# Performance work log

Hardware: AMD Instinct MI355X
Metric: run time of the kernel (lower is better)

The kernel has to match this reference:

```python
import jax, jax.numpy as jnp
import numpy as np

EPS_NORM = 1e-12
BN_EPS = 1e-5

def rmsnorm(x, gamma):
    # F.normalize(x, dim=-1) * gamma * dim**0.5
    n = jnp.maximum(jnp.linalg.norm(x, axis=-1, keepdims=True), EPS_NORM)
    return x / n * gamma * np.float32(np.sqrt(x.shape[-1]))

def conv1d(x, w, pad):
    # x: (B,C,T), w: (O,I,K)
    return jax.lax.conv_general_dilated(x, w, (1,), [(pad, pad)],
                                        dimension_numbers=('NCH', 'OIH', 'NCH'))

def maxpool3(x):
    # kernel 3, stride 1, pad 1 over last axis
    return jax.lax.reduce_window(x, -jnp.inf, jax.lax.max,
                                 (1, 1, 3), (1, 1, 1), [(0, 0), (0, 0), (1, 1)])

def gelu(x):
    return jax.nn.gelu(x, approximate=False)  # matches torch F.gelu default


def setup_inputs() -> dict:
    key = jax.random.key(0)
    ks = jax.random.split(key, 16)
    B, N, D, E, H, NF = 4, 4096, 512, 4, 1024, 32
    s = 0.02
    inp = {
        'x': jax.random.normal(ks[0], (B, N, D), jnp.float32),
        'left_k': 2048,
        'gamma1': jnp.ones((D,), jnp.float32),
        'gamma2': jnp.ones((D,), jnp.float32),
        'attn_w': jax.random.normal(ks[1], (D, 1), jnp.float32) * s,
        'attn_b': jnp.zeros((1,), jnp.float32),
        'gate_w': jax.random.normal(ks[2], (D, E), jnp.float32) * s,
        'expert_w1': jax.random.normal(ks[3], (E, D, H), jnp.float32) * s,
        'expert_w2': jax.random.normal(ks[4], (E, H, D), jnp.float32) * s,
        'bott_w': jax.random.normal(ks[5], (NF, D, 1), jnp.float32) * s,
        'conv_w39': jax.random.normal(ks[6], (NF, NF, 39), jnp.float32) * s,
        'conv_w19': jax.random.normal(ks[7], (NF, NF, 19), jnp.float32) * s,
        'conv_w9': jax.random.normal(ks[8], (NF, NF, 9), jnp.float32) * s,
        'mp_w': jax.random.normal(ks[9], (NF, D, 1), jnp.float32) * s,
        'bn_g': jnp.ones((NF * 4,), jnp.float32),
        'bn_b': jnp.zeros((NF * 4,), jnp.float32),
        'proj_w': jax.random.normal(ks[10], (NF * 4, D), jnp.float32) * s,
        'proj_b': jnp.zeros((D,), jnp.float32),
    }
    return inp


def reference(x, left_k, gamma1, gamma2, attn_w, attn_b, gate_w,
              expert_w1, expert_w2, bott_w, conv_w39, conv_w19, conv_w9,
              mp_w, bn_g, bn_b, proj_w, proj_b):
    B, N, D = x.shape
    E = gate_w.shape[-1]

    x_n = rmsnorm(x, gamma1)
    scores = jax.nn.sigmoid(x_n @ attn_w + attn_b)            # (B,N,1)
    xs = x_n * scores                                          # (B,N,D)

    # top-k token selection (remain_ratio < 1 path)
    _, top_idx = jax.lax.top_k(scores[..., 0], left_k)         # (B,left_k)
    sorted_idx = jnp.sort(top_idx, axis=1)
    left_x = jnp.take_along_axis(xs, sorted_idx[..., None], axis=1)
    # complement sum via scatter mask (faithful to scatter_/gather/sum)
    sel = jnp.zeros((B, N), x.dtype).at[jnp.arange(B)[:, None], sorted_idx].set(1.0)
    extra = jnp.einsum('bn,bnd->bd', 1.0 - sel, xs)[:, None, :]
    xcat = jnp.concatenate([left_x, extra], axis=1)            # (B,left_k+1,D)

    x_n2 = rmsnorm(xcat, gamma2)

    # dense soft MoE
    gate = jax.nn.softmax(x_n2 @ gate_w, axis=-1)              # (B,T,E)
    h = gelu(jnp.einsum('btd,edh->bteh', x_n2, expert_w1))
    eo = jnp.einsum('bteh,ehd->bted', h, expert_w2)
    moe_out = jnp.einsum('bte,bted->btd', gate, eo)
    moe_loss = E * jnp.sum(jnp.mean(gate, axis=(0, 1)) ** 2)

    # Inception branch (channels-first)
    xc = jnp.transpose(x_n2, (0, 2, 1))                        # (B,D,T)
    xb = conv1d(xc, bott_w, 0)                                 # (B,32,T)
    outs = [conv1d(xb, conv_w39, 19), conv1d(xb, conv_w19, 9),
            conv1d(xb, conv_w9, 4), conv1d(maxpool3(xc), mp_w, 0)]
    cat = jnp.concatenate(outs, axis=1)                        # (B,128,T)
    mu = jnp.mean(cat, axis=(0, 2), keepdims=True)
    var = jnp.var(cat, axis=(0, 2), keepdims=True)
    bn = (cat - mu) / jnp.sqrt(var + BN_EPS) * bn_g[None, :, None] + bn_b[None, :, None]
    incep = gelu(bn)
    incep_out = jnp.transpose(incep, (0, 2, 1)) @ proj_w + proj_b  # (B,T,D)

    out = xcat + moe_out + incep_out
    return gelu(out), moe_loss
```

## Files before the change

kernel.cpp:

```cpp
#include <hip/hip_runtime.h>
#include <hip/hip_bf16.h>
#include <math.h>

#define DEV __device__ __forceinline__

constexpr int B_ = 4, N_ = 4096, D_ = 512, E_ = 4, H_ = 1024, NF_ = 32;
constexpr int KL_ = 2048, T_ = KL_ + 1;
constexpr int TOK_ = B_ * T_;
constexpr int SP_ = 2304;

typedef __bf16 bf16x8 __attribute__((ext_vector_type(8)));
typedef float f32x4 __attribute__((ext_vector_type(4)));

DEV float gelu_f(float x){
  float t = __expf(-1.702f * x);
  return x * __builtin_amdgcn_rcpf(1.0f + t);
}
DEV float bf2f(unsigned short u){ union{unsigned int i; float f;} c; c.i = (unsigned)u << 16; return c.f; }
DEV unsigned pack2(float a, float b){
  __hip_bfloat16 ha = __float2bfloat16(a), hb = __float2bfloat16(b);
  unsigned short ua = *(unsigned short*)&ha, ub = *(unsigned short*)&hb;
  return (unsigned)ua | ((unsigned)ub << 16);
}

DEV float wave_sum(float v){
  #pragma unroll
  for (int off = 32; off > 0; off >>= 1) v += __shfl_down(v, off, 64);
  return v;
}

DEV float block_sum256(float v, float* sm){
  v = wave_sum(v);
  int lane = threadIdx.x & 63, wid = threadIdx.x >> 6;
  if (lane == 0) sm[wid] = v;
  __syncthreads();
  if (threadIdx.x == 0) sm[0] = sm[0] + sm[1] + sm[2] + sm[3];
  __syncthreads();
  float r = sm[0];
  __syncthreads();
  return r;
}

__global__ void k_rms_score(const float* __restrict__ x, const float* __restrict__ g,
                            const float* __restrict__ aw, const float* __restrict__ ab,
                            float* __restrict__ scores, float* __restrict__ scale){
  __shared__ float sm[4];
  int row = blockIdx.x; int tid = threadIdx.x;
  const float* xr = x + (size_t)row * D_;
  float v0 = xr[tid], v1 = xr[tid + 256];
  float ss = block_sum256(v0 * v0 + v1 * v1, sm);
  float a  = block_sum256(v0 * g[tid] * aw[tid] + v1 * g[tid + 256] * aw[tid + 256], sm);
  float n = fmaxf(sqrtf(ss), 1e-12f);
  float inv = 22.627416997969522f / n;
  float z = inv * a + ab[0];
  float s = 1.0f / (1.0f + expf(-z));
  if (tid == 0){ scores[row] = s; scale[row] = inv * s; }
}

__global__ void k_select(const float* __restrict__ scores, int* __restrict__ flags){
  __shared__ float s[N_];
  __shared__ int cnts[4][64];
  int b = blockIdx.y; int tid = threadIdx.x;
  int tile = blockIdx.x * 64;
  const float4* src = (const float4*)(scores + (size_t)b * N_);
  for (int j = tid; j < N_ / 4; j += 256) ((float4*)s)[j] = src[j];
  __syncthreads();
  int tok = tid & 63, part = tid >> 6;
  int i = tile + tok;
  float si = s[i];
  int cnt = 0;
  const float4* sp = (const float4*)(s + part * 1024);
  int jb = part * 1024;
  #pragma unroll 4
  for (int j = 0; j < 256; j++){
    float4 v = sp[j];
    int j4 = jb + j * 4;
    cnt += (v.x > si) || (v.x == si && (j4 + 0) < i);
    cnt += (v.y > si) || (v.y == si && (j4 + 1) < i);
    cnt += (v.z > si) || (v.z == si && (j4 + 2) < i);
    cnt += (v.w > si) || (v.w == si && (j4 + 3) < i);
  }
  cnts[part][tok] = cnt;
  __syncthreads();
  if (tid < 64){
    int c = cnts[0][tid] + cnts[1][tid] + cnts[2][tid] + cnts[3][tid];
    flags[(size_t)b * N_ + tile + tid] = (c < KL_) ? 1 : 0;
  }
}

__global__ void k_compact(const int* __restrict__ flags, int* __restrict__ idx){
  __shared__ int wsum[4];
  int b = blockIdx.x; int tid = threadIdx.x;
  const int* fb = flags + (size_t)b * N_;
  int f[16]; int cnt = 0;
  #pragma unroll
  for (int i = 0; i < 16; i++){ f[i] = fb[tid * 16 + i]; cnt += f[i]; }
  int lane = tid & 63, wid = tid >> 6;
  int v = cnt;
  #pragma unroll
  for (int off = 1; off < 64; off <<= 1){
    int t = __shfl_up(v, off, 64);
    if (lane >= off) v += t;
  }
  if (lane == 63) wsum[wid] = v;
  __syncthreads();
  int base = v - cnt;
  for (int w = 0; w < wid; w++) base += wsum[w];
  int* ib = idx + (size_t)b * KL_;
  #pragma unroll
  for (int i = 0; i < 16; i++){
    if (f[i]) ib[base++] = tid * 16 + i;
  }
}

DEV void rms2_tail(int row, float xc0, float xc1,
                   const float* __restrict__ g2, const float* __restrict__ gw,
                   __hip_bfloat16* __restrict__ xcatb,
                   __hip_bfloat16* __restrict__ xn2b, float* __restrict__ gate,
                   float* sm, float* sg){
  int tid = threadIdx.x;
  __hip_bfloat16* xb = xcatb + (size_t)row * D_;
  xb[tid] = __float2bfloat16(xc0); xb[tid + 256] = __float2bfloat16(xc1);
  float ss = block_sum256(xc0 * xc0 + xc1 * xc1, sm);
  float n = fmaxf(sqrtf(ss), 1e-12f);
  float inv = 22.627416997969522f / n;
  float xn0 = xc0 * inv * g2[tid], xn1 = xc1 * inv * g2[tid + 256];
  __hip_bfloat16* ob = xn2b + (size_t)row * D_;
  ob[tid] = __float2bfloat16(xn0); ob[tid + 256] = __float2bfloat16(xn1);
  const float4* gw4 = (const float4*)gw;
  float4 wa = gw4[tid], wb = gw4[tid + 256];
  float l0 = xn0 * wa.x + xn1 * wb.x, l1 = xn0 * wa.y + xn1 * wb.y;
  float l2 = xn0 * wa.z + xn1 * wb.z, l3 = xn0 * wa.w + xn1 * wb.w;
  l0 = wave_sum(l0); l1 = wave_sum(l1); l2 = wave_sum(l2); l3 = wave_sum(l3);
  int lane = tid & 63, wid = tid >> 6;
  if (lane == 0){ sg[wid*4+0]=l0; sg[wid*4+1]=l1; sg[wid*4+2]=l2; sg[wid*4+3]=l3; }
  __syncthreads();
  if (tid == 0){
    float a0 = sg[0]+sg[4]+sg[8]+sg[12];
    float a1 = sg[1]+sg[5]+sg[9]+sg[13];
    float a2 = sg[2]+sg[6]+sg[10]+sg[14];
    float a3 = sg[3]+sg[7]+sg[11]+sg[15];
    float m = fmaxf(fmaxf(a0, a1), fmaxf(a2, a3));
    float e0 = expf(a0-m), e1 = expf(a1-m), e2 = expf(a2-m), e3 = expf(a3-m);
    float is = 1.f / (e0+e1+e2+e3);
    float* gr = gate + (size_t)row * 4;
    gr[0]=e0*is; gr[1]=e1*is; gr[2]=e2*is; gr[3]=e3*is;
  }
}

__global__ void k_gatherrms(const float* __restrict__ x, const float* __restrict__ scale,
                            const float* __restrict__ g1, const float* __restrict__ g2,
                            const float* __restrict__ gw, const int* __restrict__ idx,
                            __hip_bfloat16* __restrict__ xcatb,
                            __hip_bfloat16* __restrict__ xn2b, float* __restrict__ gate){
  __shared__ float sm[4];
  __shared__ float sg[16];
  int rid = blockIdx.x;
  int b = rid >> 11, p = rid & (KL_ - 1);
  int tid = threadIdx.x;
  int tok = idx[(size_t)b * KL_ + p];
  float sc = scale[(size_t)b * N_ + tok];
  const float* xr = x + ((size_t)b * N_ + tok) * D_;
  float xc0 = xr[tid] * sc * g1[tid];
  float xc1 = xr[tid + 256] * sc * g1[tid + 256];
  rms2_tail(b * T_ + p, xc0, xc1, g2, gw, xcatb, xn2b, gate, sm, sg);
}

__global__ void k_extra1(const float* __restrict__ x, const float* __restrict__ scale,
                         const int* __restrict__ flags, float* __restrict__ part){
  int b = blockIdx.y, blk = blockIdx.x;
  int tid = threadIdx.x;
  const int* fb = flags + (size_t)b * N_ + blk * 64;
  const float* sb = scale + (size_t)b * N_ + blk * 64;
  const float2* xp = (const float2*)(x + ((size_t)b * N_ + blk * 64) * D_) + tid;
  float2 acc = {0.f, 0.f};
  for (int i = 0; i < 64; i++){
    if (!fb[i]){
      float s = sb[i];
      float2 v = xp[(size_t)i * 256];
      acc.x += v.x * s; acc.y += v.y * s;
    }
  }
  float* pr = part + ((size_t)(b * 64 + blk)) * D_;
  pr[tid * 2] = acc.x; pr[tid * 2 + 1] = acc.y;
}

__global__ void k_extra2r(const float* __restrict__ part, const float* __restrict__ g1,
                          const float* __restrict__ g2, const float* __restrict__ gw,
                          __hip_bfloat16* __restrict__ xcatb,
                          __hip_bfloat16* __restrict__ xn2b, float* __restrict__ gate){
  __shared__ float sm[4];
  __shared__ float sg[16];
  int b = blockIdx.x; int tid = threadIdx.x;
  float s0 = 0.f, s1 = 0.f;
  for (int i = 0; i < 64; i++){
    const float* pr = part + ((size_t)(b * 64 + i)) * D_;
    s0 += pr[tid]; s1 += pr[tid + 256];
  }
  float xc0 = s0 * g1[tid], xc1 = s1 * g1[tid + 256];
  rms2_tail(b * T_ + KL_, xc0, xc1, g2, gw, xcatb, xn2b, gate, sm, sg);
}

__global__ void k_gsumloss(const float* __restrict__ gate, float* __restrict__ o){
  __shared__ float sm[16];
  int tid = threadIdx.x;
  float4 a = {0.f, 0.f, 0.f, 0.f};
  for (int r = tid; r < TOK_; r += 256){
    float4 v = *(const float4*)(gate + (size_t)r * 4);
    a.x += v.x; a.y += v.y; a.z += v.z; a.w += v.w;
  }
  a.x = wave_sum(a.x); a.y = wave_sum(a.y); a.z = wave_sum(a.z); a.w = wave_sum(a.w);
  int lane = tid & 63, wid = tid >> 6;
  if (lane == 0){ sm[wid*4]=a.x; sm[wid*4+1]=a.y; sm[wid*4+2]=a.z; sm[wid*4+3]=a.w; }
  __syncthreads();
  if (tid == 0){
    float l = 0.f;
    #pragma unroll
    for (int e = 0; e < 4; e++){
      float s = sm[e] + sm[4+e] + sm[8+e] + sm[12+e];
      float m = s / (float)TOK_;
      l += m * m;
    }
    o[0] = (float)E_ * l;
  }
}

DEV void trb_tile(const float* __restrict__ in, __hip_bfloat16* __restrict__ out,
                  int R, int C, int bx, int by){
  __shared__ float t[32][33];
  int c0 = bx * 32, r0 = by * 32;
  int j = threadIdx.x & 31, i4 = threadIdx.x >> 5;
  #pragma unroll
  for (int k = 0; k < 4; k++){
    int i = i4 * 4 + k;
    t[i][j] = in[(size_t)(r0 + i) * C + c0 + j];
  }
  __syncthreads();
  #pragma unroll
  for (int k = 0; k < 4; k++){
    int i = i4 * 4 + k;
    out[(size_t)(c0 + i) * R + r0 + j] = __float2bfloat16(t[j][i]);
  }
}

__global__ void k_wprep(const float* __restrict__ ew1, const float* __restrict__ ew2,
                        const float* __restrict__ proj_w,
                        const float* __restrict__ w39, const float* __restrict__ w19,
                        const float* __restrict__ w9,
                        __hip_bfloat16* __restrict__ w1b, __hip_bfloat16* __restrict__ w2b,
                        __hip_bfloat16* __restrict__ projb, __hip_bfloat16* __restrict__ wcb,
                        float* __restrict__ stats){
  int blk = blockIdx.x;
  int tid = threadIdx.x;
  if (blk < 2048){
    int e = blk >> 9, rem = blk & 511;
    int by = rem >> 5, bx = rem & 31;
    trb_tile(ew1 + (size_t)e * D_ * H_, w1b + (size_t)e * D_ * H_, D_, H_, bx, by);
  } else if (blk < 4096){
    int r = blk - 2048;
    int e = r >> 9, r2 = r & 511;
    int bx = r2 & 15, by = r2 >> 4;
    __shared__ float t[32][33];
    const float* ip = ew2 + (size_t)e * H_ * D_;
    __hip_bfloat16* op = w2b + (size_t)e * H_;
    int c0 = bx * 32, r0 = by * 32;
    int j = tid & 31, i4 = tid >> 5;
    #pragma unroll
    for (int k = 0; k < 4; k++){
      int i = i4 * 4 + k;
      t[i][j] = ip[(size_t)(r0 + i) * D_ + c0 + j];
    }
    __syncthreads();
    #pragma unroll
    for (int k = 0; k < 4; k++){
      int i = i4 * 4 + k;
      int v = r0 + j;
      int pv = (v & ~63) | ((v & 15) << 2) | ((v >> 4) & 3);
      op[(size_t)(c0 + i) * 4096 + pv] = __float2bfloat16(t[j][i]);
    }
  } else if (blk < 4160){
    int r = blk - 4096;
    trb_tile(proj_w, projb, 128, D_, r & 15, r >> 4);
  } else if (blk < 4448){
    int i = (blk - 4160) * 256 + tid;
    if (i < 73728){
      const float* w; int KP, KW, base;
      if (i < 40960){ w = w39; KP = 40; KW = 39; base = 0; }
      else if (i < 61440){ w = w19; KP = 20; KW = 19; base = 40960; }
      else { w = w9; KP = 12; KW = 9; base = 61440; }
      int li = i - base;
      int oc = li / (32 * KP);
      int rem = li % (32 * KP);
      int k = rem >> 5, ic = rem & 31;
      float v = (k < KW) ? w[((size_t)oc * 32 + ic) * KW + k] : 0.f;
      wcb[i] = __float2bfloat16(v);
    }
  } else {
    stats[tid] = 0.f;
  }
}

template<int EPI>
__launch_bounds__(512)
__global__ void gemm_bt(const __hip_bfloat16* __restrict__ A,
                        const __hip_bfloat16* __restrict__ Bt,
                        __hip_bfloat16* __restrict__ Cb, size_t zstride,
                        int M, int N, int K, int kloc,
                        const float* __restrict__ gatep){
  __shared__ __align__(16) char smem[2][24576];
  int tid = threadIdx.x;
  unsigned gx = gridDim.x;
  unsigned nwg = gx * gridDim.y;
  unsigned orig = blockIdx.x + gx * blockIdx.y;
  unsigned q = nwg >> 3, r = nwg & 7;
  unsigned xcd = orig & 7, loc = orig >> 3;
  unsigned wg = (xcd < r ? xcd * (q + 1) : r * (q + 1) + (xcd - r) * q) + loc;
  int m0 = (int)(wg / gx) * 256, n0 = (int)(wg % gx) * 128;
  int z = blockIdx.z;
  int koff = z * kloc;
  int ln = tid & 63, wid = tid >> 6;
  int wm = wid >> 1, wn = wid & 1;

  f32x4 acc[4][4] = {};

  auto stage = [&](int buf, int k0){
    #pragma unroll
    for (int c = 0; c < 2; c++){
      int ii = tid + c * 512;
      int rr = ii >> 2, s = ii & 3;
      int gm = m0 + rr; gm = gm < M ? gm : M - 1;
      const __hip_bfloat16* gp = A + (size_t)gm * K + (koff + k0 + ((s ^ (rr & 3)) << 3));
      __builtin_amdgcn_global_load_lds(
          (const __attribute__((address_space(1))) void*)gp,
          (__attribute__((address_space(3))) void*)&smem[buf][ii * 16], 16, 0, 0);
    }
    {
      int ii = tid;
      int rr = ii >> 2, s = ii & 3;
      const __hip_bfloat16* gp = Bt + (size_t)(n0 + rr) * K + (koff + k0 + ((s ^ (rr & 3)) << 3));
      __builtin_amdgcn_global_load_lds(
          (const __attribute__((address_space(1))) void*)gp,
          (__attribute__((address_space(3))) void*)&smem[buf][16384 + ii * 16], 16, 0, 0);
    }
  };

  int nk = kloc >> 5;
  stage(0, 0);
  __syncthreads();
  int slotb = (((ln >> 4) ^ (ln & 3)) << 4);
  for (int t = 0; t < nk; t++){
    int buf = t & 1;
    if (t + 1 < nk) stage(buf ^ 1, (t + 1) << 5);
    bf16x8 af[4], bfr[4];
    #pragma unroll
    for (int m = 0; m < 4; m++){
      int R = wm * 64 + m * 16 + (ln & 15);
      af[m] = *(const bf16x8*)&smem[buf][R * 64 + slotb];
    }
    #pragma unroll
    for (int n = 0; n < 4; n++){
      int R = wn * 64 + n * 16 + (ln & 15);
      bfr[n] = *(const bf16x8*)&smem[buf][16384 + R * 64 + slotb];
    }
    #pragma unroll
    for (int m = 0; m < 4; m++)
      #pragma unroll
      for (int n = 0; n < 4; n++)
        acc[m][n] = __builtin_amdgcn_mfma_f32_16x16x32_bf16(af[m], bfr[n], acc[m][n], 0, 0, 0);
    __syncthreads();
  }

  __hip_bfloat16* Co = Cb + (size_t)z * zstride;
  int e = n0 >> 10;
  int lr = ln & 15;
  #pragma unroll
  for (int m = 0; m < 4; m++){
    int rb = m0 + wm * 64 + m * 16 + ((ln >> 4) << 2);
    float gv[4];
    if (EPI == 1){
      #pragma unroll
      for (int r2 = 0; r2 < 4; r2++)
        gv[r2] = (rb + r2 < M) ? gatep[(size_t)(rb + r2) * 4 + e] : 0.f;
    }
    #pragma unroll
    for (int r2 = 0; r2 < 4; r2++){
      int row = rb + r2;
      if (row < M){
        float v0 = acc[m][0][r2], v1 = acc[m][1][r2];
        float v2 = acc[m][2][r2], v3 = acc[m][3][r2];
        if (EPI == 1){
          v0 = gelu_f(v0) * gv[r2]; v1 = gelu_f(v1) * gv[r2];
          v2 = gelu_f(v2) * gv[r2]; v3 = gelu_f(v3) * gv[r2];
        }
        uint2 pk; pk.x = pack2(v0, v1); pk.y = pack2(v2, v3);
        size_t ci = (size_t)row * N + (n0 + wn * 64 + 4 * lr);
        *(uint2*)&Co[ci] = pk;
      }
    }
  }
}

__global__ void k_1x1F(const __hip_bfloat16* __restrict__ xn2b, const float* __restrict__ bw,
                       const float* __restrict__ mw,
                       __hip_bfloat16* __restrict__ xbp, float* __restrict__ cat){
  __shared__ float Xs[32 * 65];
  __shared__ float Ws[64 * 36];
  int type = blockIdx.y;
  const float* w = type == 0 ? bw : mw;
  int tid = threadIdx.x;
  int G0 = blockIdx.x * 32;
  int tok = tid & 31, grp = tid >> 5;
  float acc[4] = {};
  for (int d0 = 0; d0 < D_; d0 += 64){
    #pragma unroll
    for (int j = tid; j < 512; j += 256){
      int tt = j >> 4, dc = (j & 15) * 4;
      int g = G0 + tt;
      float4 v = {0.f, 0.f, 0.f, 0.f};
      if (g < TOK_){
        const __hip_bfloat16* p = xn2b + (size_t)g * D_ + d0 + dc;
        ushort4 rw = *(const ushort4*)p;
        v.x = bf2f(rw.x); v.y = bf2f(rw.y); v.z = bf2f(rw.z); v.w = bf2f(rw.w);
        if (type == 1){
          int t = g % T_;
          if (t > 0){
            ushort4 u = *(const ushort4*)(p - D_);
            v.x = fmaxf(v.x, bf2f(u.x)); v.y = fmaxf(v.y, bf2f(u.y));
            v.z = fmaxf(v.z, bf2f(u.z)); v.w = fmaxf(v.w, bf2f(u.w));
          }
          if (t < T_ - 1){
            ushort4 u = *(const ushort4*)(p + D_);
            v.x = fmaxf(v.x, bf2f(u.x)); v.y = fmaxf(v.y, bf2f(u.y));
            v.z = fmaxf(v.z, bf2f(u.z)); v.w = fmaxf(v.w, bf2f(u.w));
          }
        }
      }
      float* xd = &Xs[tt * 65 + dc];
      xd[0] = v.x; xd[1] = v.y; xd[2] = v.z; xd[3] = v.w;
    }
    #pragma unroll
    for (int j = tid; j < 2048; j += 256){
      int f = j >> 6, d = j & 63;
      Ws[d * 36 + f] = w[(size_t)f * D_ + d0 + d];
    }
    __syncthreads();
    const float* xr = &Xs[tok * 65];
    #pragma unroll 8
    for (int d = 0; d < 64; d++){
      float xv = xr[d];
      const float4* w4 = (const float4*)&Ws[d * 36 + grp * 4];
      float4 a = w4[0];
      acc[0] += xv * a.x; acc[1] += xv * a.y; acc[2] += xv * a.z; acc[3] += xv * a.w;
    }
    __syncthreads();
  }
  int g = G0 + tok;
  if (g < TOK_){
    if (type == 0){
      int bb = g / T_, t = g % T_;
      __hip_bfloat16* op = xbp + ((size_t)(bb * SP_ + 32 + t)) * 32 + grp * 4;
      #pragma unroll
      for (int j = 0; j < 4; j++) op[j] = __float2bfloat16(acc[j]);
    } else {
      float* op = cat + (size_t)g * 128 + 96 + grp * 4;
      #pragma unroll
      for (int j = 0; j < 4; j++) op[j] = acc[j];
    }
  }
}

template<int KP, int PAD, int OFF, int TYPE>
DEV void convm_body(const __hip_bfloat16* __restrict__ xbp,
                    const __hip_bfloat16* __restrict__ wcb,
                    float* __restrict__ cat, char* smem){
  constexpr int R = KP * 32;
  int t0 = blockIdx.x * 128, b = blockIdx.y;
  int tid = threadIdx.x;
  for (int j = tid; j < 768; j += 256){
    int r = j >> 2, c = j & 3;
    int rg = b * SP_ + 32 + t0 - PAD + r;
    const __hip_bfloat16* gp = xbp + (size_t)rg * 32 + ((c ^ (r & 3)) << 3);
    __builtin_amdgcn_global_load_lds(
        (const __attribute__((address_space(1))) void*)gp,
        (__attribute__((address_space(3))) void*)(smem + j * 16), 16, 0, 0);
  }
  __syncthreads();
  int ln = tid & 63, wid = tid >> 6;
  int lr = ln & 15, lg = ln >> 4;
  int tb = wid * 32;
  const __hip_bfloat16* wt = wcb + OFF;
  const __hip_bfloat16* bp0 = wt + (size_t)lr * R + lg * 8;
  const __hip_bfloat16* bp1 = wt + (size_t)(16 + lr) * R + lg * 8;
  f32x4 acc[2][2] = {};
  bf16x8 bc0 = *(const bf16x8*)bp0;
  bf16x8 bc1 = *(const bf16x8*)bp1;
  #pragma unroll 4
  for (int s = 0; s < KP; s++){
    bf16x8 bn0 = bc0, bn1 = bc1;
    if (s + 1 < KP){
      bn0 = *(const bf16x8*)(bp0 + (s + 1) * 32);
      bn1 = *(const bf16x8*)(bp1 + (s + 1) * 32);
    }
    int ra0 = tb + lr + s;
    int ra1 = tb + 16 + lr + s;
    bf16x8 a0 = *(const bf16x8*)(smem + ra0 * 64 + ((lg ^ (ra0 & 3)) << 4));
    bf16x8 a1 = *(const bf16x8*)(smem + ra1 * 64 + ((lg ^ (ra1 & 3)) << 4));
    acc[0][0] = __builtin_amdgcn_mfma_f32_16x16x32_bf16(a0, bc0, acc[0][0], 0, 0, 0);
    acc[0][1] = __builtin_amdgcn_mfma_f32_16x16x32_bf16(a0, bc1, acc[0][1], 0, 0, 0);
    acc[1][0] = __builtin_amdgcn_mfma_f32_16x16x32_bf16(a1, bc0, acc[1][0], 0, 0, 0);
    acc[1][1] = __builtin_amdgcn_mfma_f32_16x16x32_bf16(a1, bc1, acc[1][1], 0, 0, 0);
    bc0 = bn0; bc1 = bn1;
  }
  #pragma unroll
  for (int m = 0; m < 2; m++){
    int rb = tb + m * 16 + (lg << 2);
    #pragma unroll
    for (int n = 0; n < 2; n++){
      int oc = n * 16 + lr;
      #pragma unroll
      for (int j2 = 0; j2 < 4; j2++){
        int tp = t0 + rb + j2;
        if (tp < T_)
          cat[((size_t)b * T_ + tp) * 128 + TYPE * 32 + oc] = acc[m][n][j2];
      }
    }
  }
}

__global__ __launch_bounds__(256)
void k_convM(const __hip_bfloat16* __restrict__ xbp,
             const __hip_bfloat16* __restrict__ wcb, float* __restrict__ cat){
  __shared__ __align__(16) char smem[192 * 64];
  if (blockIdx.z == 0)      convm_body<40, 19, 0,     0>(xbp, wcb, cat, smem);
  else if (blockIdx.z == 1) convm_body<20, 9,  40960, 1>(xbp, wcb, cat, smem);
  else                      convm_body<12, 4,  61440, 2>(xbp, wcb, cat, smem);
}

__global__ void k_bnstat(const float* __restrict__ cat, float* __restrict__ stats){
  __shared__ float sm[512];
  int tid = threadIdx.x;
  float s = 0.f, q = 0.f;
  for (int rp = blockIdx.x; rp < TOK_ / 2; rp += gridDim.x){
    float v = cat[(size_t)rp * 256 + tid];
    s += v; q += v * v;
  }
  sm[tid] = s; sm[256 + tid] = q;
  __syncthreads();
  if (tid < 128){
    atomicAdd(&stats[tid], sm[tid] + sm[tid + 128]);
    atomicAdd(&stats[128 + tid], sm[256 + tid] + sm[256 + tid + 128]);
  }
}

__global__ void k_bnact(const float* __restrict__ cat, __hip_bfloat16* __restrict__ catb,
                        const float* __restrict__ stats,
                        const float* __restrict__ g, const float* __restrict__ b){
  int i = blockIdx.x * 256 + threadIdx.x;
  int c = i & 127;
  float mu = stats[c] * (1.f / TOK_);
  float var = stats[128 + c] * (1.f / TOK_) - mu * mu;
  float v = cat[i];
  v = (v - mu) * rsqrtf(var + 1e-5f) * g[c] + b[c];
  catb[i] = __float2bfloat16(gelu_f(v));
}

__global__ void k_final(const __hip_bfloat16* __restrict__ xcatb,
                        const __hip_bfloat16* __restrict__ moeb,
                        size_t zs, const __hip_bfloat16* __restrict__ ioutb,
                        const float* __restrict__ pb, float* __restrict__ out){
  size_t i = ((size_t)blockIdx.x * 256 + threadIdx.x) * 2;
  int p = (int)(i & 511);
  size_t rowbase = i - p;
  float s0 = 0.f, s1 = 0.f;
  #pragma unroll
  for (int z = 0; z < 4; z++){
    unsigned u = *(const unsigned*)&moeb[(size_t)z * zs + i];
    s0 += bf2f((unsigned short)(u & 0xffff));
    s1 += bf2f((unsigned short)(u >> 16));
  }
  unsigned v = *(const unsigned*)&ioutb[i];
  s0 += bf2f((unsigned short)(v & 0xffff));
  s1 += bf2f((unsigned short)(v >> 16));
  int d0 = (p & ~63) | ((p & 3) << 4) | ((p >> 2) & 15);
  int p1 = p + 1;
  int d1 = (p1 & ~63) | ((p1 & 3) << 4) | ((p1 >> 2) & 15);
  const unsigned short* xc = (const unsigned short*)xcatb;
  s0 += bf2f(xc[rowbase + d0]) + pb[d0];
  s1 += bf2f(xc[rowbase + d1]) + pb[d1];
  out[rowbase + d0] = gelu_f(s0);
  out[rowbase + d1] = gelu_f(s1);
}

extern "C" void kernel_launch(void* const* d_in, const int* in_sizes, int n_in,
                              void* d_out, int out_size, void* d_ws, size_t ws_size,
                              hipStream_t stream){
  const float* x      = (const float*)d_in[0];
  const float* gamma1 = (const float*)d_in[2];
  const float* gamma2 = (const float*)d_in[3];
  const float* attn_w = (const float*)d_in[4];
  const float* attn_b = (const float*)d_in[5];
  const float* gate_w = (const float*)d_in[6];
  const float* ew1    = (const float*)d_in[7];
  const float* ew2    = (const float*)d_in[8];
  const float* bott_w = (const float*)d_in[9];
  const float* w39    = (const float*)d_in[10];
  const float* w19    = (const float*)d_in[11];
  const float* w9     = (const float*)d_in[12];
  const float* mp_w   = (const float*)d_in[13];
  const float* bn_g   = (const float*)d_in[14];
  const float* bn_b   = (const float*)d_in[15];
  const float* proj_w = (const float*)d_in[16];
  const float* proj_b = (const float*)d_in[17];
  float* out = (float*)d_out;

  float* ws = (float*)d_ws;
  size_t off = 0;
  auto alloc = [&](size_t n){ size_t o = off; off += (n + 63) & ~(size_t)63; return o; };
  size_t f_hb   = alloc((size_t)TOK_ * 4096 / 2);
  size_t f_sc   = alloc(B_ * N_);
  size_t f_sca  = alloc(B_ * N_);
  size_t f_fl   = alloc(B_ * N_);
  size_t f_idx  = alloc(B_ * KL_);
  size_t f_xcb  = alloc((size_t)TOK_ * D_ / 2 + 64);
  size_t f_moeb = alloc((size_t)4 * TOK_ * D_ / 2 + 64);
  size_t f_gate = alloc(TOK_ * E_);
  size_t f_st   = alloc(256);
  size_t f_xbp  = alloc((size_t)B_ * SP_ * 32 / 2);
  size_t f_cat  = alloc((size_t)TOK_ * 128);
  size_t f_wb   = alloc((size_t)(E_ * D_ * H_) + (size_t)TOK_ * D_ / 2 + 64);
  size_t f_part = alloc((size_t)B_ * 64 * D_);
  size_t f_wcb  = alloc(73728 / 2 + 64);
  size_t f_pjb  = alloc(512 * 128 / 2 + 64);
  (void)ws_size; (void)in_sizes; (void)n_in; (void)out_size;

  float* sc   = ws + f_sc;
  float* sca  = ws + f_sca;
  int*   fl   = (int*)(ws + f_fl);
  int*   idx  = (int*)(ws + f_idx);
  float* gate = ws + f_gate;
  float* stats= ws + f_st;
  float* cat  = ws + f_cat;
  float* part = ws + f_part;
  __hip_bfloat16* xcatb = (__hip_bfloat16*)(ws + f_xcb);
  __hip_bfloat16* moeb  = (__hip_bfloat16*)(ws + f_moeb);
  __hip_bfloat16* xbp   = (__hip_bfloat16*)(ws + f_xbp);
  __hip_bfloat16* wcb   = (__hip_bfloat16*)(ws + f_wcb);
  __hip_bfloat16* projb = (__hip_bfloat16*)(ws + f_pjb);
  __hip_bfloat16* hbuf  = (__hip_bfloat16*)(ws + f_hb);
  __hip_bfloat16* ioutb = (__hip_bfloat16*)(ws + f_hb);
  __hip_bfloat16* catb  = (__hip_bfloat16*)(ws + f_hb + 4196416);
  __hip_bfloat16* w1b  = (__hip_bfloat16*)(ws + f_wb);
  __hip_bfloat16* w2b  = w1b + (size_t)E_ * D_ * H_;
  __hip_bfloat16* xn2b = w2b + (size_t)E_ * D_ * H_;

  hipMemsetAsync(xbp, 0, (size_t)B_ * SP_ * 32 * sizeof(__hip_bfloat16), stream);

  k_wprep<<<4449, 256, 0, stream>>>(ew1, ew2, proj_w, w39, w19, w9,
                                    w1b, w2b, projb, wcb, stats);

  k_rms_score<<<B_ * N_, 256, 0, stream>>>(x, gamma1, attn_w, attn_b, sc, sca);
  k_select<<<dim3(N_ / 64, B_), 256, 0, stream>>>(sc, fl);
  k_compact<<<B_, 256, 0, stream>>>(fl, idx);
  k_gatherrms<<<B_ * KL_, 256, 0, stream>>>(x, sca, gamma1, gamma2, gate_w, idx,
                                            xcatb, xn2b, gate);
  k_extra1<<<dim3(64, B_), 256, 0, stream>>>(x, sca, fl, part);
  k_extra2r<<<B_, 256, 0, stream>>>(part, gamma1, gamma2, gate_w, xcatb, xn2b, gate);
  k_gsumloss<<<1, 256, 0, stream>>>(gate, out + (size_t)TOK_ * D_);

  int mt = (TOK_ + 255) / 256;
  size_t zs = (size_t)TOK_ * D_;
  gemm_bt<1><<<dim3(4096/128, mt), 512, 0, stream>>>(
      xn2b, w1b, hbuf, 0, TOK_, 4096, D_, D_, gate);
  gemm_bt<0><<<dim3(D_/128, mt, 4), 512, 0, stream>>>(
      hbuf, w2b, moeb, zs, TOK_, D_, 4096, 1024, nullptr);

  int t32 = (TOK_ + 31) / 32;
  k_1x1F<<<dim3(t32, 2), 256, 0, stream>>>(xn2b, bott_w, mp_w, xbp, cat);
  k_convM<<<dim3(17, 4, 3), 256, 0, stream>>>(xbp, wcb, cat);
  k_bnstat<<<256, 256, 0, stream>>>(cat, stats);
  k_bnact<<<(TOK_ * 128) / 256, 256, 0, stream>>>(cat, catb, stats, bn_g, bn_b);
  gemm_bt<0><<<dim3(D_/128, mt), 512, 0, stream>>>(
      catb, projb, ioutb, 0, TOK_, D_, 128, 128, nullptr);
  k_final<<<((size_t)TOK_ * D_) / 512, 256, 0, stream>>>(xcatb, moeb, zs, ioutb, proj_b, out);
}
```

Baseline: 297.3 us.

## Move 1x1 bottleneck and maxpool convs onto MFMA with separate pool kernel

Replaces the scalar fp32 shared-memory 1x1 conv kernel with a bf16 MFMA kernel that double-buffers 128-token tiles through LDS via direct global-to-LDS loads. The 3-wide maxpool is split into its own kernel that writes a pooled bf16 copy of the normalized input, and the 1x1 weights are pre-converted to bf16 in the weight-prep kernel. This targets the FMA-bound scalar loop. In exchange it adds an extra launch and a full activation-sized round trip through memory for the pooled tensor.

```diff
diff --git a/kernel.cpp b/kernel.cpp
--- a/kernel.cpp
+++ b/kernel.cpp
@@ -247,9 +247,10 @@
                         const float* __restrict__ proj_w,
                         const float* __restrict__ w39, const float* __restrict__ w19,
                         const float* __restrict__ w9,
+                        const float* __restrict__ bott_w, const float* __restrict__ mp_w,
                         __hip_bfloat16* __restrict__ w1b, __hip_bfloat16* __restrict__ w2b,
                         __hip_bfloat16* __restrict__ projb, __hip_bfloat16* __restrict__ wcb,
-                        float* __restrict__ stats){
+                        __hip_bfloat16* __restrict__ wb1x1, float* __restrict__ stats){
   int blk = blockIdx.x;
   int tid = threadIdx.x;
   if (blk < 2048){
@@ -295,6 +296,10 @@
       float v = (k < KW) ? w[((size_t)oc * 32 + ic) * KW + k] : 0.f;
       wcb[i] = __float2bfloat16(v);
     }
+  } else if (blk < 4576){
+    int i = (blk - 4448) * 256 + tid;
+    const float* w = (i < 16384) ? bott_w : mp_w;
+    wb1x1[i] = __float2bfloat16(w[i & 16383]);
   } else {
     stats[tid] = 0.f;
   }
@@ -400,71 +405,94 @@
   }
 }
 
-__global__ void k_1x1F(const __hip_bfloat16* __restrict__ xn2b, const float* __restrict__ bw,
-                       const float* __restrict__ mw,
-                       __hip_bfloat16* __restrict__ xbp, float* __restrict__ cat){
-  __shared__ float Xs[32 * 65];
-  __shared__ float Ws[64 * 36];
+__global__ void k_pool(const unsigned* __restrict__ xin, unsigned* __restrict__ xout){
+  size_t i = (size_t)blockIdx.x * 256 + threadIdx.x;
+  if (i >= (size_t)TOK_ * 256) return;
+  int g = (int)(i >> 8);
+  int t = g % T_;
+  unsigned c = xin[i];
+  float a0 = bf2f((unsigned short)(c & 0xffff)), a1 = bf2f((unsigned short)(c >> 16));
+  if (t > 0){
+    unsigned u = xin[i - 256];
+    a0 = fmaxf(a0, bf2f((unsigned short)(u & 0xffff)));
+    a1 = fmaxf(a1, bf2f((unsigned short)(u >> 16)));
+  }
+  if (t < T_ - 1){
+    unsigned u = xin[i + 256];
+    a0 = fmaxf(a0, bf2f((unsigned short)(u & 0xffff)));
+    a1 = fmaxf(a1, bf2f((unsigned short)(u >> 16)));
+  }
+  xout[i] = pack2(a0, a1);
+}
+
+__global__ __launch_bounds__(256)
+void k_1x1M(const __hip_bfloat16* __restrict__ xn2b, const __hip_bfloat16* __restrict__ xn2mb,
+            const __hip_bfloat16* __restrict__ wb1x1,
+            __hip_bfloat16* __restrict__ xbp, float* __restrict__ cat){
+  __shared__ __align__(16) char smem[2][16384];
   int type = blockIdx.y;
-  const float* w = type == 0 ? bw : mw;
-  int tid = threadIdx.x;
-  int G0 = blockIdx.x * 32;
-  int tok = tid & 31, grp = tid >> 5;
-  float acc[4] = {};
-  for (int d0 = 0; d0 < D_; d0 += 64){
-    #pragma unroll
-    for (int j = tid; j < 512; j += 256){
-      int tt = j >> 4, dc = (j & 15) * 4;
-      int g = G0 + tt;
-      float4 v = {0.f, 0.f, 0.f, 0.f};
-      if (g < TOK_){
-        const __hip_bfloat16* p = xn2b + (size_t)g * D_ + d0 + dc;
-        ushort4 rw = *(const ushort4*)p;
-        v.x = bf2f(rw.x); v.y = bf2f(rw.y); v.z = bf2f(rw.z); v.w = bf2f(rw.w);
-        if (type == 1){
-          int t = g % T_;
-          if (t > 0){
-            ushort4 u = *(const ushort4*)(p - D_);
-            v.x = fmaxf(v.x, bf2f(u.x)); v.y = fmaxf(v.y, bf2f(u.y));
-            v.z = fmaxf(v.z, bf2f(u.z)); v.w = fmaxf(v.w, bf2f(u.w));
-          }
-          if (t < T_ - 1){
-            ushort4 u = *(const ushort4*)(p + D_);
-            v.x = fmaxf(v.x, bf2f(u.x)); v.y = fmaxf(v.y, bf2f(u.y));
-            v.z = fmaxf(v.z, bf2f(u.z)); v.w = fmaxf(v.w, bf2f(u.w));
+  const __hip_bfloat16* A = type ? xn2mb : xn2b;
+  const __hip_bfloat16* W = wb1x1 + (size_t)type * 32 * 512;
+  int t0 = blockIdx.x * 128;
+  int tid = threadIdx.x, ln = tid & 63, wid = tid >> 6;
+  int lr = ln & 15, lg = ln >> 4;
+
+  auto stage = [&](int buf, int k0){
+    #pragma unroll
+    for (int c = 0; c < 4; c++){
+      int ii = tid + c * 256;
+      int r = ii >> 3, s = ii & 7;
+      int row = t0 + r; row = row < TOK_ ? row : TOK_ - 1;
+      const __hip_bfloat16* gp = A + (size_t)row * D_ + k0 + ((s ^ (r & 7)) << 3);
+      __builtin_amdgcn_global_load_lds(
+          (const __attribute__((address_space(1))) void*)gp,
+          (__attribute__((address_space(3))) void*)&smem[buf][ii * 16], 16, 0, 0);
+    }
+  };
+
+  f32x4 acc[2][2] = {};
+  stage(0, 0);
+  __syncthreads();
+  for (int t = 0; t < 8; t++){
+    int buf = t & 1;
+    if (t + 1 < 8) stage(buf ^ 1, (t + 1) * 64);
+    int k0 = t * 64;
+    #pragma unroll
+    for (int kk = 0; kk < 2; kk++){
+      bf16x8 bfr[2];
+      #pragma unroll
+      for (int n = 0; n < 2; n++)
+        bfr[n] = *(const bf16x8*)&W[(size_t)(n * 16 + lr) * 512 + k0 + kk * 32 + lg * 8];
+      #pragma unroll
+      for (int m = 0; m < 2; m++){
+        int R = wid * 32 + m * 16 + lr;
+        int phys = (kk * 4 + lg) ^ (R & 7);
+        bf16x8 af = *(const bf16x8*)&smem[buf][R * 128 + phys * 16];
+        acc[m][0] = __builtin_amdgcn_mfma_f32_16x16x32_bf16(af, bfr[0], acc[m][0], 0, 0, 0);
+        acc[m][1] = __builtin_amdgcn_mfma_f32_16x16x32_bf16(af, bfr[1], acc[m][1], 0, 0, 0);
+      }
+    }
+    __syncthreads();
+  }
+  #pragma unroll
+  for (int m = 0; m < 2; m++){
+    int rb = t0 + wid * 32 + m * 16 + lg * 4;
+    #pragma unroll
+    for (int n = 0; n < 2; n++){
+      int oc = n * 16 + lr;
+      #pragma unroll
+      for (int r2 = 0; r2 < 4; r2++){
+        int g = rb + r2;
+        if (g < TOK_){
+          float v = acc[m][n][r2];
+          if (type == 0){
+            int bb = g / T_, t = g % T_;
+            xbp[((size_t)(bb * SP_ + 32 + t)) * 32 + oc] = __float2bfloat16(v);
+          } else {
+            cat[(size_t)g * 128 + 96 + oc] = v;
           }
         }
       }
-      float* xd = &Xs[tt * 65 + dc];
-      xd[0] = v.x; xd[1] = v.y; xd[2] = v.z; xd[3] = v.w;
-    }
-    #pragma unroll
-    for (int j = tid; j < 2048; j += 256){
-      int f = j >> 6, d = j & 63;
-      Ws[d * 36 + f] = w[(size_t)f * D_ + d0 + d];
-    }
-    __syncthreads();
-    const float* xr = &Xs[tok * 65];
-    #pragma unroll 8
-    for (int d = 0; d < 64; d++){
-      float xv = xr[d];
-      const float4* w4 = (const float4*)&Ws[d * 36 + grp * 4];
-      float4 a = w4[0];
-      acc[0] += xv * a.x; acc[1] += xv * a.y; acc[2] += xv * a.z; acc[3] += xv * a.w;
-    }
-    __syncthreads();
-  }
-  int g = G0 + tok;
-  if (g < TOK_){
-    if (type == 0){
-      int bb = g / T_, t = g % T_;
-      __hip_bfloat16* op = xbp + ((size_t)(bb * SP_ + 32 + t)) * 32 + grp * 4;
-      #pragma unroll
-      for (int j = 0; j < 4; j++) op[j] = __float2bfloat16(acc[j]);
-    } else {
-      float* op = cat + (size_t)g * 128 + 96 + grp * 4;
-      #pragma unroll
-      for (int j = 0; j < 4; j++) op[j] = acc[j];
     }
   }
 }
@@ -626,11 +654,13 @@
   size_t f_gate = alloc(TOK_ * E_);
   size_t f_st   = alloc(256);
   size_t f_xbp  = alloc((size_t)B_ * SP_ * 32 / 2);
+  size_t f_xmb  = alloc((size_t)TOK_ * D_ / 2 + 64);
   size_t f_cat  = alloc((size_t)TOK_ * 128);
   size_t f_wb   = alloc((size_t)(E_ * D_ * H_) + (size_t)TOK_ * D_ / 2 + 64);
   size_t f_part = alloc((size_t)B_ * 64 * D_);
   size_t f_wcb  = alloc(73728 / 2 + 64);
   size_t f_pjb  = alloc(512 * 128 / 2 + 64);
+  size_t f_w11  = alloc(32768 / 2 + 64);
   (void)ws_size; (void)in_sizes; (void)n_in; (void)out_size;
 
   float* sc   = ws + f_sc;
@@ -644,8 +674,10 @@
   __hip_bfloat16* xcatb = (__hip_bfloat16*)(ws + f_xcb);
   __hip_bfloat16* moeb  = (__hip_bfloat16*)(ws + f_moeb);
   __hip_bfloat16* xbp   = (__hip_bfloat16*)(ws + f_xbp);
+  __hip_bfloat16* xn2mb = (__hip_bfloat16*)(ws + f_xmb);
   __hip_bfloat16* wcb   = (__hip_bfloat16*)(ws + f_wcb);
   __hip_bfloat16* projb = (__hip_bfloat16*)(ws + f_pjb);
+  __hip_bfloat16* wb1x1 = (__hip_bfloat16*)(ws + f_w11);
   __hip_bfloat16* hbuf  = (__hip_bfloat16*)(ws + f_hb);
   __hip_bfloat16* ioutb = (__hip_bfloat16*)(ws + f_hb);
   __hip_bfloat16* catb  = (__hip_bfloat16*)(ws + f_hb + 4196416);
@@ -655,8 +687,8 @@
 
   hipMemsetAsync(xbp, 0, (size_t)B_ * SP_ * 32 * sizeof(__hip_bfloat16), stream);
 
-  k_wprep<<<4449, 256, 0, stream>>>(ew1, ew2, proj_w, w39, w19, w9,
-                                    w1b, w2b, projb, wcb, stats);
+  k_wprep<<<4577, 256, 0, stream>>>(ew1, ew2, proj_w, w39, w19, w9, bott_w, mp_w,
+                                    w1b, w2b, projb, wcb, wb1x1, stats);
 
   k_rms_score<<<B_ * N_, 256, 0, stream>>>(x, gamma1, attn_w, attn_b, sc, sca);
   k_select<<<dim3(N_ / 64, B_), 256, 0, stream>>>(sc, fl);
@@ -674,8 +706,9 @@
   gemm_bt<0><<<dim3(D_/128, mt, 4), 512, 0, stream>>>(
       hbuf, w2b, moeb, zs, TOK_, D_, 4096, 1024, nullptr);
 
-  int t32 = (TOK_ + 31) / 32;
-  k_1x1F<<<dim3(t32, 2), 256, 0, stream>>>(xn2b, bott_w, mp_w, xbp, cat);
+  int t128 = (TOK_ + 127) / 128;
+  k_pool<<<(TOK_ * 256 + 255) / 256, 256, 0, stream>>>((const unsigned*)xn2b, (unsigned*)xn2mb);
+  k_1x1M<<<dim3(t128, 2), 256, 0, stream>>>(xn2b, xn2mb, wb1x1, xbp, cat);
   k_convM<<<dim3(17, 4, 3), 256, 0, stream>>>(xbp, wcb, cat);
   k_bnstat<<<256, 256, 0, stream>>>(cat, stats);
   k_bnact<<<(TOK_ * 128) / 256, 256, 0, stream>>>(cat, catb, stats, bn_g, bn_b);
```

Measured after the change: 276.9 us. 6.9% less time.
